# Optimization experiments

Hardware: AMD Instinct MI355X
Metric: run time of the kernel (lower is better)

The kernel has to match this reference:

```python
import jax, jax.numpy as jnp
import numpy as np

B, S, D_IN, D_OUT = 4, 4096, 512, 512


def setup_inputs() -> dict:
    key = jax.random.key(0)
    k1, k2, k3, k4 = jax.random.split(key, 4)
    sc = 1.0 / np.sqrt(D_IN)
    return {
        "x": jax.random.normal(k1, (B, S, D_IN), dtype=jnp.float32),
        "Wq": jax.random.normal(k2, (D_OUT, D_IN), dtype=jnp.float32) * sc,
        "Wk": jax.random.normal(k3, (D_OUT, D_IN), dtype=jnp.float32) * sc,
        "Wv": jax.random.normal(k4, (D_OUT, D_IN), dtype=jnp.float32) * sc,
    }


def reference(x, Wq, Wk, Wv):
    # nn.Linear: y = x @ W.T  (no bias)
    q = jnp.einsum("bsd,ed->bse", x, Wq)  # [B,S,D_OUT]
    k = jnp.einsum("bsd,ed->bse", x, Wk)
    v = jnp.einsum("bsd,ed->bse", x, Wv)
    scale = 1.0 / jnp.sqrt(jnp.asarray(k.shape[-1], dtype=x.dtype))
    scores = jnp.einsum("bqe,bke->bqk", q, k) * scale  # [B,S,S]
    # causal mask: position q attends to k <= q
    s = x.shape[1]
    causal = jnp.tril(jnp.ones((s, s), dtype=bool))
    scores = jnp.where(causal[None, :, :], scores, -jnp.inf)
    attn = jax.nn.softmax(scores, axis=-1)
    # dropout p=0.0 -> identity
    return jnp.einsum("bqk,bke->bqe", attn, v)  # [B,S,D_OUT]
```

## Files before the change

### kernel.cpp

```cpp
#include <hip/hip_runtime.h>

typedef __attribute__((ext_vector_type(8))) short short8;
typedef __attribute__((ext_vector_type(4))) float f32x4;

#define GLD_AS1 const __attribute__((address_space(1))) void*
#define GLD_AS3 __attribute__((address_space(3))) void*

__device__ __forceinline__ unsigned short f2bf(float f) {
  unsigned u = __builtin_bit_cast(unsigned, f);
  u += 0x7fffu + ((u >> 16) & 1u);
  return (unsigned short)(u >> 16);
}
__device__ __forceinline__ float bf2f(unsigned short h) {
  return __builtin_bit_cast(float, (unsigned)h << 16);
}

__global__ void cvt_f32_bf16(const float* __restrict__ in, unsigned short* __restrict__ out, int n4) {
  int i = blockIdx.x * blockDim.x + threadIdx.x;
  const int st = gridDim.x * blockDim.x;
  for (; i < n4; i += st) {
    float4 f = reinterpret_cast<const float4*>(in)[i];
    unsigned long long p = (unsigned long long)f2bf(f.x)
        | ((unsigned long long)f2bf(f.y) << 16)
        | ((unsigned long long)f2bf(f.z) << 32)
        | ((unsigned long long)f2bf(f.w) << 48);
    reinterpret_cast<unsigned long long*>(out)[i] = p;
  }
}

__global__ void cvt_w3(const float* __restrict__ wq, const float* __restrict__ wk,
                       const float* __restrict__ wv, unsigned short* __restrict__ wcat) {
  const int n4 = 3 * 65536;
  int i = blockIdx.x * blockDim.x + threadIdx.x;
  const int st = gridDim.x * blockDim.x;
  for (; i < n4; i += st) {
    const int seg = i >> 16, off = i & 65535;
    const float* src = (seg == 0) ? wq : (seg == 1) ? wk : wv;
    float4 f = reinterpret_cast<const float4*>(src)[off];
    unsigned long long p = (unsigned long long)f2bf(f.x)
        | ((unsigned long long)f2bf(f.y) << 16)
        | ((unsigned long long)f2bf(f.z) << 32)
        | ((unsigned long long)f2bf(f.w) << 48);
    reinterpret_cast<unsigned long long*>(wcat)[i] = p;
  }
}

__global__ __launch_bounds__(256) void qkv_gemm(
    const unsigned short* __restrict__ xb, const unsigned short* __restrict__ wcat,
    unsigned short* __restrict__ qb, unsigned short* __restrict__ kb,
    unsigned short* __restrict__ vtb) {
  __shared__ unsigned short As[128 * 64];
  __shared__ unsigned short Bs[128 * 64];
  const int tid = threadIdx.x, lane = tid & 63, w = tid >> 6;
  const int m0 = blockIdx.y * 128, n0 = blockIdx.x * 128;
  const int wr = w >> 1, wc = w & 1;
  const float QSCALE = 0.0637587085f;

  f32x4 acc[4][4];
  const f32x4 z4 = {0.f, 0.f, 0.f, 0.f};
  #pragma unroll
  for (int a = 0; a < 4; ++a)
    #pragma unroll
    for (int c = 0; c < 4; ++c) acc[a][c] = z4;

  for (int it = 0; it < 8; ++it) {
    const int k0 = it * 64;
    #pragma unroll
    for (int c = 0; c < 4; ++c) {
      const int rbase = 32 * w + 8 * c;
      const int r = rbase + (lane >> 3);
      const int c16 = (lane & 7) ^ (r & 7);
      const unsigned short* ga = xb + (size_t)(m0 + r) * 512 + k0 + c16 * 8;
      const unsigned short* gb = wcat + (size_t)(n0 + r) * 512 + k0 + c16 * 8;
      __builtin_amdgcn_global_load_lds((GLD_AS1)ga, (GLD_AS3)&As[rbase * 64], 16, 0, 0);
      __builtin_amdgcn_global_load_lds((GLD_AS1)gb, (GLD_AS3)&Bs[rbase * 64], 16, 0, 0);
    }
    __syncthreads();
    #pragma unroll
    for (int ks = 0; ks < 2; ++ks) {
      const int ck = ks * 4 + (lane >> 4);
      short8 av[4], bv[4];
      #pragma unroll
      for (int fr = 0; fr < 4; ++fr) {
        const int rl = 64 * wr + 16 * fr + (lane & 15);
        av[fr] = *reinterpret_cast<const short8*>(&As[rl * 64 + ((ck ^ (rl & 7)) << 3)]);
      }
      #pragma unroll
      for (int fc = 0; fc < 4; ++fc) {
        const int rl = 64 * wc + 16 * fc + (lane & 15);
        bv[fc] = *reinterpret_cast<const short8*>(&Bs[rl * 64 + ((ck ^ (rl & 7)) << 3)]);
      }
      #pragma unroll
      for (int fr = 0; fr < 4; ++fr)
        #pragma unroll
        for (int fc = 0; fc < 4; ++fc)
          acc[fr][fc] = __builtin_amdgcn_mfma_f32_16x16x32_bf16(av[fr], bv[fc], acc[fr][fc], 0, 0, 0);
    }
    __syncthreads();
  }

  const int which = n0 >> 9;
  #pragma unroll
  for (int fr = 0; fr < 4; ++fr) {
    #pragma unroll
    for (int fc = 0; fc < 4; ++fc) {
      const int n = n0 + 64 * wc + 16 * fc + (lane & 15);
      const int nl = n & 511;
      #pragma unroll
      for (int j = 0; j < 4; ++j) {
        const int m = m0 + 64 * wr + 16 * fr + (lane >> 4) * 4 + j;
        const float a = acc[fr][fc][j];
        const unsigned short v = f2bf(which == 0 ? a * QSCALE : a);
        if (which == 0)      qb[(size_t)m * 512 + nl] = v;
        else if (which == 1) kb[(size_t)m * 512 + nl] = v;
        else                 vtb[((size_t)((m >> 12) * 512 + nl)) * 4096 + (m & 4095)] = v;
      }
    }
  }
}

__global__ __launch_bounds__(512, 2) void attn_fwd(
    const unsigned short* __restrict__ qg, const unsigned short* __restrict__ kg,
    const unsigned short* __restrict__ vtg,
    float* __restrict__ out0,
    unsigned short* __restrict__ out1,
    float* __restrict__ ml) {
  __shared__ __align__(16) unsigned short Ks[2][64 * 512];
  __shared__ __align__(16) unsigned short P_lds[64][72];
  __shared__ __align__(16) float psums[2][64];

  const int tid = threadIdx.x, lane = tid & 63, w = tid >> 6;
  const int idx = blockIdx.x;
  const int qt = 63 - (idx >> 3);
  const int b = (idx >> 1) & 3;
  const int half = idx & 1;
  const int nkt = qt + 1;
  const int kt0 = half ? (nkt >> 1) : 0;
  const int kt1 = half ? nkt : (nkt >> 1);
  const int q0 = qt * 64;

  const unsigned short* Qb  = qg  + (size_t)b * 4096 * 512;
  const unsigned short* Kb  = kg  + (size_t)b * 4096 * 512;
  const unsigned short* Vtb = vtg + (size_t)b * 512 * 4096;

  const int wr = w & 3, wc = w >> 2, g = lane >> 4, dw = w * 64;
  const int rbase = 16 * wr + 4 * g;

  short8 qreg[16];
  {
    const unsigned short* qrow = Qb + (size_t)(q0 + 16 * wr + (lane & 15)) * 512 + (lane >> 4) * 8;
    #pragma unroll
    for (int ks = 0; ks < 16; ++ks)
      qreg[ks] = *reinterpret_cast<const short8*>(qrow + ks * 32);
  }

  const f32x4 z4 = {0.f, 0.f, 0.f, 0.f};
  f32x4 oacc[4][4];
  #pragma unroll
  for (int fr = 0; fr < 4; ++fr)
    #pragma unroll
    for (int fc = 0; fc < 4; ++fc) oacc[fr][fc] = z4;

  float l_run[4];
  #pragma unroll
  for (int j = 0; j < 4; ++j) l_run[j] = 0.f;

  short8 vreg[2][4];
  f32x4 sacc_cur[2], sacc_nxt[2];

#define STAGE_K(kt_, buf_) do {                                                          \
    _Pragma("unroll")                                                                    \
    for (int r8 = 0; r8 < 8; ++r8) {                                                     \
      const int r_ = r8 * 8 + w;                                                         \
      const unsigned short* g_ = Kb + (size_t)((kt_) * 64 + r_) * 512 + (lane ^ (r_ & 7)) * 8; \
      __builtin_amdgcn_global_load_lds((GLD_AS1)g_, (GLD_AS3)&Ks[buf_][r_ * 512], 16, 0, 0);   \
    }                                                                                    \
  } while (0)

#define QK_TILE(buf_, S_) do {                                                           \
    _Pragma("unroll")                                                                    \
    for (int ks = 0; ks < 16; ++ks) {                                                    \
      const int ck = ks * 4 + (lane >> 4);                                               \
      _Pragma("unroll")                                                                  \
      for (int fc = 0; fc < 2; ++fc) {                                                   \
        const int rl = 32 * wc + 16 * fc + (lane & 15);                                  \
        const short8 bv = *reinterpret_cast<const short8*>(                              \
            &Ks[buf_][rl * 512 + ((ck ^ (rl & 7)) << 3)]);                               \
        S_[fc] = __builtin_amdgcn_mfma_f32_16x16x32_bf16(qreg[ks], bv, S_[fc], 0, 0, 0); \
      }                                                                                  \
    }                                                                                    \
  } while (0)

#define PV_STEP() do {                                                                   \
    _Pragma("unroll")                                                                    \
    for (int ks = 0; ks < 2; ++ks) {                                                     \
      short8 av[4];                                                                      \
      _Pragma("unroll")                                                                  \
      for (int fr = 0; fr < 4; ++fr)                                                     \
        av[fr] = *reinterpret_cast<const short8*>(                                       \
            &P_lds[16 * fr + (lane & 15)][ks * 32 + (lane >> 4) * 8]);                   \
      __builtin_amdgcn_s_setprio(1);                                                     \
      _Pragma("unroll")                                                                  \
      for (int fr = 0; fr < 4; ++fr)                                                     \
        _Pragma("unroll")                                                                \
        for (int fc = 0; fc < 4; ++fc)                                                   \
          oacc[fr][fc] = __builtin_amdgcn_mfma_f32_16x16x32_bf16(av[fr], vreg[ks][fc],   \
                                                                 oacc[fr][fc], 0, 0, 0);\
      __builtin_amdgcn_s_setprio(0);                                                     \
    }                                                                                    \
  } while (0)

  if (kt0 < kt1) {
    STAGE_K(kt0, 0);
    if (kt0 + 1 < kt1) STAGE_K(kt0 + 1, 1);
    __syncthreads();
    sacc_cur[0] = z4; sacc_cur[1] = z4;
    QK_TILE(0, sacc_cur);
    __syncthreads();

    int cur = 0;
    for (int t = kt0; t < kt1; ++t, cur ^= 1) {
      if (t + 2 < kt1) STAGE_K(t + 2, cur);
      if (t > kt0) PV_STEP();
      if (t == qt) {
        #pragma unroll
        for (int fc = 0; fc < 2; ++fc) {
          const int col = 32 * wc + 16 * fc + (lane & 15);
          #pragma unroll
          for (int j = 0; j < 4; ++j)
            if (col > rbase + j) sacc_cur[fc][j] = -1e30f;
        }
      }
      __syncthreads();

      const int kv0 = t * 64;
      #pragma unroll
      for (int ks = 0; ks < 2; ++ks)
        #pragma unroll
        for (int fc = 0; fc < 4; ++fc)
          vreg[ks][fc] = *reinterpret_cast<const short8*>(
              Vtb + (size_t)(dw + 16 * fc + (lane & 15)) * 4096 + kv0 + ks * 32 + (lane >> 4) * 8);
      {
        const int colb = 32 * wc + (lane & 15);
        #pragma unroll
        for (int j = 0; j < 4; ++j) {
          const float p0 = __builtin_amdgcn_exp2f(sacc_cur[0][j]);
          const float p1 = __builtin_amdgcn_exp2f(sacc_cur[1][j]);
          l_run[j] += p0 + p1;
          P_lds[rbase + j][colb]      = f2bf(p0);
          P_lds[rbase + j][colb + 16] = f2bf(p1);
        }
      }
      if (t + 1 < kt1) {
        sacc_nxt[0] = z4; sacc_nxt[1] = z4;
        __builtin_amdgcn_s_setprio(1);
        QK_TILE(cur ^ 1, sacc_nxt);
        __builtin_amdgcn_s_setprio(0);
        sacc_cur[0] = sacc_nxt[0]; sacc_cur[1] = sacc_nxt[1];
      }
      __syncthreads();
    }
    PV_STEP();
  }

  #pragma unroll
  for (int j = 0; j < 4; ++j) {
    l_run[j] += __shfl_xor(l_run[j], 1);
    l_run[j] += __shfl_xor(l_run[j], 2);
    l_run[j] += __shfl_xor(l_run[j], 4);
    l_run[j] += __shfl_xor(l_run[j], 8);
  }
  if ((lane & 15) == 0) {
    f32x4 l4 = {l_run[0], l_run[1], l_run[2], l_run[3]};
    *reinterpret_cast<f32x4*>(&psums[wc][rbase]) = l4;
  }
  __syncthreads();
  if ((lane & 15) == 0 && wc == 0) {
    const int rg = b * 4096 + q0 + rbase;
    const f32x4 la = *reinterpret_cast<const f32x4*>(&psums[0][rbase]);
    const f32x4 lb = *reinterpret_cast<const f32x4*>(&psums[1][rbase]);
    f32x4 m4 = {0.f, 0.f, 0.f, 0.f};
    f32x4 l4 = {la[0] + lb[0], la[1] + lb[1], la[2] + lb[2], la[3] + lb[3]};
    *reinterpret_cast<f32x4*>(&ml[(half * 2) * 16384 + rg])     = m4;
    *reinterpret_cast<f32x4*>(&ml[(half * 2 + 1) * 16384 + rg]) = l4;
  }
  if (half == 0) {
    float* ob = out0 + (size_t)b * 4096 * 512;
    #pragma unroll
    for (int fr = 0; fr < 4; ++fr)
      #pragma unroll
      for (int j = 0; j < 4; ++j) {
        const int row = 16 * fr + (lane >> 4) * 4 + j;
        #pragma unroll
        for (int fc = 0; fc < 4; ++fc)
          ob[(size_t)(q0 + row) * 512 + dw + 16 * fc + (lane & 15)] = oacc[fr][fc][j];
      }
  } else {
    unsigned short* ob = out1 + (size_t)b * 4096 * 512;
    #pragma unroll
    for (int fr = 0; fr < 4; ++fr)
      #pragma unroll
      for (int j = 0; j < 4; ++j) {
        const int row = 16 * fr + (lane >> 4) * 4 + j;
        #pragma unroll
        for (int fc = 0; fc < 4; ++fc)
          ob[(size_t)(q0 + row) * 512 + dw + 16 * fc + (lane & 15)] = f2bf(oacc[fr][fc][j]);
      }
  }
#undef STAGE_K
#undef QK_TILE
#undef PV_STEP
}

__global__ void attn_merge(float* __restrict__ out, const unsigned short* __restrict__ o1,
                           const float* __restrict__ ml) {
  const int total = 16384 * 128;
  int i = blockIdx.x * blockDim.x + threadIdx.x;
  const int st = gridDim.x * blockDim.x;
  for (; i < total; i += st) {
    const int r = i >> 7;
    const float m0 = ml[r], l0 = ml[16384 + r];
    const float m1 = ml[2 * 16384 + r], l1 = ml[3 * 16384 + r];
    const float m = fmaxf(m0, m1);
    const float a0 = __builtin_amdgcn_exp2f(m0 - m), a1 = __builtin_amdgcn_exp2f(m1 - m);
    const float inv = 1.0f / (a0 * l0 + a1 * l1);
    const float s0 = a0 * inv, s1 = a1 * inv;
    float4 v0 = reinterpret_cast<const float4*>(out)[i];
    ushort4 v1 = reinterpret_cast<const ushort4*>(o1)[i];
    float4 o;
    o.x = v0.x * s0 + bf2f(v1.x) * s1;
    o.y = v0.y * s0 + bf2f(v1.y) * s1;
    o.z = v0.z * s0 + bf2f(v1.z) * s1;
    o.w = v0.w * s0 + bf2f(v1.w) * s1;
    reinterpret_cast<float4*>(out)[i] = o;
  }
}

extern "C" void kernel_launch(void* const* d_in, const int* in_sizes, int n_in,
                              void* d_out, int out_size, void* d_ws, size_t ws_size,
                              hipStream_t stream) {
  const float* x  = (const float*)d_in[0];
  const float* wq = (const float*)d_in[1];
  const float* wk = (const float*)d_in[2];
  const float* wv = (const float*)d_in[3];

  char* ws = (char*)d_ws;
  unsigned short* xb   = (unsigned short*)(ws);
  unsigned short* wcat = (unsigned short*)(ws + (16u << 20));
  float*          mlp  = (float*)(ws + (18u << 20));
  unsigned short* qb   = (unsigned short*)(ws + (20u << 20));
  unsigned short* kb   = (unsigned short*)(ws + (36u << 20));
  unsigned short* vtb  = (unsigned short*)(ws + (52u << 20));

  cvt_f32_bf16<<<2048, 256, 0, stream>>>(x, xb, (4 * 4096 * 512) / 4);
  cvt_w3<<<768, 256, 0, stream>>>(wq, wk, wv, wcat);

  qkv_gemm<<<dim3(12, 128), 256, 0, stream>>>(xb, wcat, qb, kb, vtb);

  attn_fwd<<<512, 512, 0, stream>>>(qb, kb, vtb, (float*)d_out, xb, mlp);
  attn_merge<<<2048, 256, 0, stream>>>((float*)d_out, xb, mlp);
}
```

Baseline: 210.8 us.

## Double-buffer P tile and replace syncthreads with partial-vmcnt barriers

The softmax probability tile in shared memory is now double-buffered by key-tile parity. That removes one of the two block-wide barriers per key iteration. The remaining barrier uses an explicit s_waitcnt vmcnt(8) plus s_barrier, so the next V register loads can stay in flight across it instead of draining every outstanding global load. The V loads move after the P writes, and the K buffer index is now derived from the tile index. The cost is more LDS for the second P buffer and hand-written wait counts that depend on the exact number of outstanding loads.

After: 203.8 us. 3.3% less time.

```diff
diff --git a/kernel.cpp b/kernel.cpp
--- a/kernel.cpp
+++ b/kernel.cpp
@@ -119,6 +119,12 @@
   }
 }
 
+#define FENCE() __builtin_amdgcn_sched_barrier(0)
+#define BAR_VM8()  do { FENCE(); asm volatile("s_waitcnt vmcnt(8) lgkmcnt(0)" ::: "memory"); \
+                        FENCE(); __builtin_amdgcn_s_barrier(); FENCE(); } while (0)
+#define BAR_VM0()  do { FENCE(); asm volatile("s_waitcnt vmcnt(0) lgkmcnt(0)" ::: "memory"); \
+                        FENCE(); __builtin_amdgcn_s_barrier(); FENCE(); } while (0)
+
 __global__ __launch_bounds__(512, 2) void attn_fwd(
     const unsigned short* __restrict__ qg, const unsigned short* __restrict__ kg,
     const unsigned short* __restrict__ vtg,
@@ -126,7 +132,7 @@
     unsigned short* __restrict__ out1,
     float* __restrict__ ml) {
   __shared__ __align__(16) unsigned short Ks[2][64 * 512];
-  __shared__ __align__(16) unsigned short P_lds[64][72];
+  __shared__ __align__(16) unsigned short P_lds[2][64][72];
   __shared__ __align__(16) float psums[2][64];
 
   const int tid = threadIdx.x, lane = tid & 63, w = tid >> 6;
@@ -168,12 +174,12 @@
   short8 vreg[2][4];
   f32x4 sacc_cur[2], sacc_nxt[2];
 
-#define STAGE_K(kt_, buf_) do {                                                          \
+#define STAGE_K(kt_) do {                                                                \
     _Pragma("unroll")                                                                    \
     for (int r8 = 0; r8 < 8; ++r8) {                                                     \
       const int r_ = r8 * 8 + w;                                                         \
       const unsigned short* g_ = Kb + (size_t)((kt_) * 64 + r_) * 512 + (lane ^ (r_ & 7)) * 8; \
-      __builtin_amdgcn_global_load_lds((GLD_AS1)g_, (GLD_AS3)&Ks[buf_][r_ * 512], 16, 0, 0);   \
+      __builtin_amdgcn_global_load_lds((GLD_AS1)g_, (GLD_AS3)&Ks[(kt_) & 1][r_ * 512], 16, 0, 0); \
     }                                                                                    \
   } while (0)
 
@@ -191,14 +197,14 @@
     }                                                                                    \
   } while (0)
 
-#define PV_STEP() do {                                                                   \
+#define PV_STEP(pb_) do {                                                                \
     _Pragma("unroll")                                                                    \
     for (int ks = 0; ks < 2; ++ks) {                                                     \
       short8 av[4];                                                                      \
       _Pragma("unroll")                                                                  \
       for (int fr = 0; fr < 4; ++fr)                                                     \
         av[fr] = *reinterpret_cast<const short8*>(                                       \
-            &P_lds[16 * fr + (lane & 15)][ks * 32 + (lane >> 4) * 8]);                   \
+            &P_lds[pb_][16 * fr + (lane & 15)][ks * 32 + (lane >> 4) * 8]);              \
       __builtin_amdgcn_s_setprio(1);                                                     \
       _Pragma("unroll")                                                                  \
       for (int fr = 0; fr < 4; ++fr)                                                     \
@@ -211,17 +217,23 @@
   } while (0)
 
   if (kt0 < kt1) {
-    STAGE_K(kt0, 0);
-    if (kt0 + 1 < kt1) STAGE_K(kt0 + 1, 1);
-    __syncthreads();
+    STAGE_K(kt0);
+    const bool two = (kt0 + 1 < kt1);
+    if (two) STAGE_K(kt0 + 1);
+    FENCE();
+    if (two) { asm volatile("s_waitcnt vmcnt(8)" ::: "memory"); }
+    else     { asm volatile("s_waitcnt vmcnt(0)" ::: "memory"); }
+    FENCE();
+    __builtin_amdgcn_s_barrier();
+    FENCE();
     sacc_cur[0] = z4; sacc_cur[1] = z4;
-    QK_TILE(0, sacc_cur);
-    __syncthreads();
-
-    int cur = 0;
-    for (int t = kt0; t < kt1; ++t, cur ^= 1) {
-      if (t + 2 < kt1) STAGE_K(t + 2, cur);
-      if (t > kt0) PV_STEP();
+    QK_TILE(kt0 & 1, sacc_cur);
+    BAR_VM0();
+
+    for (int t = kt0; t < kt1; ++t) {
+      if (t + 2 < kt1) STAGE_K(t + 2);
+      FENCE();
+      if (t > kt0) PV_STEP((t - 1) & 1);
       if (t == qt) {
         #pragma unroll
         for (int fc = 0; fc < 2; ++fc) {
@@ -231,15 +243,6 @@
             if (col > rbase + j) sacc_cur[fc][j] = -1e30f;
         }
       }
-      __syncthreads();
-
-      const int kv0 = t * 64;
-      #pragma unroll
-      for (int ks = 0; ks < 2; ++ks)
-        #pragma unroll
-        for (int fc = 0; fc < 4; ++fc)
-          vreg[ks][fc] = *reinterpret_cast<const short8*>(
-              Vtb + (size_t)(dw + 16 * fc + (lane & 15)) * 4096 + kv0 + ks * 32 + (lane >> 4) * 8);
       {
         const int colb = 32 * wc + (lane & 15);
         #pragma unroll
@@ -247,20 +250,27 @@
           const float p0 = __builtin_amdgcn_exp2f(sacc_cur[0][j]);
           const float p1 = __builtin_amdgcn_exp2f(sacc_cur[1][j]);
           l_run[j] += p0 + p1;
-          P_lds[rbase + j][colb]      = f2bf(p0);
-          P_lds[rbase + j][colb + 16] = f2bf(p1);
+          P_lds[t & 1][rbase + j][colb]      = f2bf(p0);
+          P_lds[t & 1][rbase + j][colb + 16] = f2bf(p1);
         }
       }
+      const int kv0 = t * 64;
+      #pragma unroll
+      for (int ks = 0; ks < 2; ++ks)
+        #pragma unroll
+        for (int fc = 0; fc < 4; ++fc)
+          vreg[ks][fc] = *reinterpret_cast<const short8*>(
+              Vtb + (size_t)(dw + 16 * fc + (lane & 15)) * 4096 + kv0 + ks * 32 + (lane >> 4) * 8);
       if (t + 1 < kt1) {
         sacc_nxt[0] = z4; sacc_nxt[1] = z4;
         __builtin_amdgcn_s_setprio(1);
-        QK_TILE(cur ^ 1, sacc_nxt);
+        QK_TILE((t + 1) & 1, sacc_nxt);
         __builtin_amdgcn_s_setprio(0);
         sacc_cur[0] = sacc_nxt[0]; sacc_cur[1] = sacc_nxt[1];
       }
-      __syncthreads();
+      BAR_VM8();
     }
-    PV_STEP();
+    PV_STEP((kt1 - 1) & 1);
   }
 
   #pragma unroll
```
